# Optimization experiments

Measured on AMD Instinct MI355X. Metric: run time of the kernel, lower is better.

Reference implementation:

```python
import jax, jax.numpy as jnp
import numpy as np

B, S, D, H = 4, 2048, 1024, 16
DH = D // H  # 64

def setup_inputs() -> dict:
    key = jax.random.key(0)
    k0, k1, k2, k3 = jax.random.split(key, 4)
    x = jax.random.normal(k0, (B, S, D), dtype=jnp.float32)
    # Linear layers use random_normal init, shape (D, D), no bias.
    Wq = jax.random.normal(k1, (D, D), dtype=jnp.float32) * 0.05
    Wk = jax.random.normal(k2, (D, D), dtype=jnp.float32) * 0.05
    Wv = jax.random.normal(k3, (D, D), dtype=jnp.float32) * 0.05
    return {"encoder_input": x, "Wq": Wq, "Wk": Wk, "Wv": Wv}

def reference(encoder_input, Wq, Wk, Wv):
    x = encoder_input
    n_heads = H
    # Per-document projections, batched: [B,S,D]
    q = jnp.einsum('bsd,de->bse', x, Wq)
    k = jnp.einsum('bsd,de->bse', x, Wk)
    v = jnp.einsum('bsd,de->bse', x, Wv)
    # np.split(..., H, axis=-1) == reshape last dim to [H, DH]
    q = q.reshape(B, S, n_heads, DH)
    k = k.reshape(B, S, n_heads, DH)
    v = v.reshape(B, S, n_heads, DH)
    # Scaled dot-product attention; NOTE: original divides by N_HEADS, not sqrt(d_head)
    scores = jnp.einsum('bqhd,bkhd->bhqk', q, k) / jnp.float32(n_heads)
    attn = jax.nn.softmax(scores, axis=-1)
    out = jnp.einsum('bhqk,bkhd->bqhd', attn, v)
    # Concatenate heads along last dim -> [B,S,D]
    return out.reshape(B, S, D)
```

## Files before the change

kernel.cpp:

```cpp
#include <hip/hip_runtime.h>

typedef unsigned short u16;
typedef unsigned int   u32;
typedef __bf16 bf16x8 __attribute__((ext_vector_type(8)));
typedef __bf16 bf16x4 __attribute__((ext_vector_type(4)));
typedef float  f32x4  __attribute__((ext_vector_type(4)));
typedef u32    u32x4  __attribute__((ext_vector_type(4)));
typedef u32    u32x2  __attribute__((ext_vector_type(2)));
typedef u16    u16x8  __attribute__((ext_vector_type(8)));

#define MFMA16(a,b,c) __builtin_amdgcn_mfma_f32_16x16x32_bf16(a,b,c,0,0,0)

#define BB 4
#define SS 2048
#define DD 1024
#define HH 16
#define DH 64
#define MM 8192

#define QSCALE 0.0901684400555602f

#define WAIT_VM0() __builtin_amdgcn_s_waitcnt(0x0F70)

__device__ __forceinline__ u16 f2bf(float f) {
  u32 u = __builtin_bit_cast(u32, f);
  u += 0x7fffu + ((u >> 16) & 1u);
  return (u16)(u >> 16);
}

__device__ __forceinline__ void async16(const void* g, void* l) {
  __builtin_amdgcn_global_load_lds(
      (const __attribute__((address_space(1))) unsigned int*)g,
      (__attribute__((address_space(3))) unsigned int*)l, 16, 0, 0);
}

__global__ __launch_bounds__(256) void convert_x(
    const float* __restrict__ in, u16* __restrict__ out)
{
  const size_t stride = (size_t)gridDim.x * 256 * 8;
  for (size_t i = ((size_t)blockIdx.x * 256 + threadIdx.x) * 8;
       i < (size_t)MM * DD; i += stride) {
    f32x4 a = *(const f32x4*)(in + i);
    f32x4 b = *(const f32x4*)(in + i + 4);
    u32x2 ua = __builtin_bit_cast(u32x2, __builtin_convertvector(a, bf16x4));
    u32x2 ub = __builtin_bit_cast(u32x2, __builtin_convertvector(b, bf16x4));
    u32x4 v = {ua[0], ua[1], ub[0], ub[1]};
    *(u32x4*)(out + i) = v;
  }
}

__global__ __launch_bounds__(256) void fill_sig(float* __restrict__ out, int n)
{
  for (int i = blockIdx.x * 256 + threadIdx.x; i < n; i += gridDim.x * 256)
    out[i] = 3.0f;
}

__global__ __launch_bounds__(256) void convert_w(
    const float* __restrict__ w0, const float* __restrict__ w1,
    const float* __restrict__ w2, u16* __restrict__ WtAll)
{
  const int z = blockIdx.z;
  const float* W = (z == 0) ? w0 : ((z == 1) ? w1 : w2);
  u16* Wt = WtAll + (size_t)z * DD * DD;
  const int n0 = blockIdx.x * 64;
  const int k0 = blockIdx.y * 64;
  __shared__ u16 tile[64][65];
#pragma unroll
  for (int i = 0; i < 16; ++i) {
    int e = threadIdx.x + i * 256;
    int r = e >> 6, c = e & 63;
    tile[r][c] = f2bf(W[(size_t)(k0 + r) * DD + n0 + c]);
  }
  __syncthreads();
#pragma unroll
  for (int i = 0; i < 16; ++i) {
    int e = threadIdx.x + i * 256;
    int r = e >> 6, c = e & 63;
    Wt[(size_t)(n0 + r) * DD + k0 + c] = tile[c][r];
  }
}

__global__ __launch_bounds__(256) void qkv_gemm(
    const u16* __restrict__ X, const u16* __restrict__ WtAll,
    u16* __restrict__ QKV)
{
  const int z = blockIdx.z;
  const u16* Wt = WtAll + (size_t)z * DD * DD;
  u16* Y = QKV + (size_t)z * MM * DD;
  const int m0 = blockIdx.x * 128;
  const int n0 = blockIdx.y * 128;
  const int t = threadIdx.x;
  const int ln = t & 63;
  const int w  = t >> 6;
  const int cl = ln & 15;
  const int qd = ln >> 4;
  const int wm = (w & 1) * 64;
  const int wn = (w >> 1) * 64;
  const int srow8 = ln >> 3;
  const int sch   = (((ln & 7) ^ (srow8 & 7)) << 3);
  const int ch0   = ((qd ^ (cl & 7)) << 3);

  __shared__ __align__(16) u16 Asm[2][128 * 64];
  __shared__ __align__(16) u16 Bsm[2][128 * 64];

  const f32x4 fzero = {0.f, 0.f, 0.f, 0.f};
  f32x4 acc[4][4];
#pragma unroll
  for (int i = 0; i < 4; ++i)
#pragma unroll
    for (int j = 0; j < 4; ++j) acc[i][j] = fzero;

  auto stage = [&](int k0, int bi) {
#pragma unroll
    for (int c = 0; c < 4; ++c) {
      async16(X  + (size_t)(m0 + c * 32 + w * 8 + srow8) * DD + k0 + sch,
              &Asm[bi][(c * 32 + w * 8) * 64]);
      async16(Wt + (size_t)(n0 + c * 32 + w * 8 + srow8) * DD + k0 + sch,
              &Bsm[bi][(c * 32 + w * 8) * 64]);
    }
  };

  stage(0, 0);

  for (int k0 = 0; k0 < DD; k0 += 64) {
    const int cur = (k0 >> 6) & 1;
    WAIT_VM0();
    __syncthreads();
    if (k0 + 64 < DD) stage(k0 + 64, cur ^ 1);

    const u16* Ah = Asm[cur];
    const u16* Bh = Bsm[cur];

#pragma unroll
    for (int kk = 0; kk < 2; ++kk) {
      bf16x8 af[4], bf[4];
#pragma unroll
      for (int mb = 0; mb < 4; ++mb)
        af[mb] = *(const bf16x8*)&Ah[(wm + mb * 16 + cl) * 64 + (ch0 ^ (kk << 5))];
#pragma unroll
      for (int nb = 0; nb < 4; ++nb)
        bf[nb] = *(const bf16x8*)&Bh[(wn + nb * 16 + cl) * 64 + (ch0 ^ (kk << 5))];
#pragma unroll
      for (int mb = 0; mb < 4; ++mb)
#pragma unroll
        for (int nb = 0; nb < 4; ++nb)
          acc[mb][nb] = MFMA16(af[mb], bf[nb], acc[mb][nb]);
    }
  }

  const float scl = (z == 0) ? QSCALE : 1.0f;
#pragma unroll
  for (int mb = 0; mb < 4; ++mb) {
#pragma unroll
    for (int r = 0; r < 4; ++r) {
      const size_t row = (size_t)(m0 + wm + mb * 16 + qd * 4 + r) * DD;
      f32x4 v = {acc[mb][0][r] * scl, acc[mb][1][r] * scl,
                 acc[mb][2][r] * scl, acc[mb][3][r] * scl};
      bf16x4 bv = __builtin_convertvector(v, bf16x4);
#pragma unroll
      for (int nb = 0; nb < 4; ++nb)
        *(__bf16*)&Y[row + n0 + wn + nb * 16 + cl] = bv[nb];
    }
  }
}

__global__ __launch_bounds__(256) void vtrans(
    const u16* __restrict__ V, u16* __restrict__ VtG)
{
  const int b = blockIdx.z;
  const int h = blockIdx.y;
  const int s0 = blockIdx.x * 64;
  __shared__ u16 tile[64][65];
#pragma unroll
  for (int i = 0; i < 16; ++i) {
    int e = threadIdx.x + i * 256;
    int r = e >> 6, c = e & 63;
    tile[r][c] = V[(size_t)(b * SS + s0 + r) * DD + h * DH + c];
  }
  __syncthreads();
#pragma unroll
  for (int i = 0; i < 16; ++i) {
    int e = threadIdx.x + i * 256;
    int r = e >> 6, c = e & 63;
    int k = c & 31;
    int pos = (c & 32) + ((k & 15) >> 2) * 8 + (k >> 4) * 4 + (k & 3);
    VtG[((size_t)(b * HH + h) * DH + r) * SS + s0 + pos] = tile[c][r];
  }
}

__global__ __launch_bounds__(256, 2) void attn_kernel(
    const u16* __restrict__ QKV, const u16* __restrict__ VtG,
    float* __restrict__ Out)
{
  const int bh = blockIdx.x;
  const int b = bh >> 4;
  const int h = bh & 15;
  const int q0 = blockIdx.y * 256;
  const int t = threadIdx.x;
  const int ln = t & 63;
  const int w  = t >> 6;
  const int cl = ln & 15;
  const int qd = ln >> 4;
  const int srow = ln >> 2;
  const int swz = (((ln & 3) ^ ((srow >> 1) & 3)) << 3);
  const int sx = ((qd ^ ((cl >> 1) & 3)) << 3);

  const u16* Qg = QKV;
  const u16* Kg = QKV + (size_t)MM * DD;

  __shared__ __align__(16) u16 smem[16384];

  const size_t qoff0 = (size_t)(b * SS + q0 + w * 16 + cl) * DD + h * DH;
  const bf16x8 qf0a = *(const bf16x8*)(Qg + qoff0 + qd * 8);
  const bf16x8 qf0b = *(const bf16x8*)(Qg + qoff0 + 32 + qd * 8);
  const bf16x8 qf1a = *(const bf16x8*)(Qg + qoff0 + (size_t)64 * DD + qd * 8);
  const bf16x8 qf1b = *(const bf16x8*)(Qg + qoff0 + (size_t)64 * DD + 32 + qd * 8);
  const bf16x8 qf2a = *(const bf16x8*)(Qg + qoff0 + (size_t)128 * DD + qd * 8);
  const bf16x8 qf2b = *(const bf16x8*)(Qg + qoff0 + (size_t)128 * DD + 32 + qd * 8);
  const bf16x8 qf3a = *(const bf16x8*)(Qg + qoff0 + (size_t)192 * DD + qd * 8);
  const bf16x8 qf3b = *(const bf16x8*)(Qg + qoff0 + (size_t)192 * DD + 32 + qd * 8);

  const f32x4 fzero = {0.f, 0.f, 0.f, 0.f};
  f32x4 oacc0[4], oacc1[4], oacc2[4], oacc3[4];
#pragma unroll
  for (int mt = 0; mt < 4; ++mt) {
    oacc0[mt] = fzero; oacc1[mt] = fzero; oacc2[mt] = fzero; oacc3[mt] = fzero;
  }
  float lsum0 = 0.f, lsum1 = 0.f, lsum2 = 0.f, lsum3 = 0.f;

  const size_t kgbase  = (size_t)b * SS * DD + (size_t)h * DH;
  const size_t vtgbase = ((size_t)(b * HH + h)) * DH * SS;

  auto stage = [&](int kt, int bi) {
    u16* kb = smem + bi * 4096;
    u16* vb = smem + 8192 + bi * 4096;
#pragma unroll
    for (int s = 0; s < 2; ++s) {
      async16(Kg  + kgbase + (size_t)(kt + w * 16 + srow) * DD + s * 32 + swz,
              kb + (s * 64 + w * 16) * 32);
      async16(VtG + vtgbase + (size_t)(w * 16 + srow) * SS + kt + s * 32 + swz,
              vb + (s * 64 + w * 16) * 32);
    }
  };

#define PAIR(QA0, QA1, QB0, QB1, OA, OB, LA, LB) do {                         \
    f32x4 stA[4], stB[4];                                                     \
    _Pragma("unroll")                                                         \
    for (int mt = 0; mt < 4; ++mt) {                                          \
      f32x4 za = fzero, zb = fzero;                                           \
      za = MFMA16(kf0[mt], QA0, za); za = MFMA16(kf1[mt], QA1, za);           \
      zb = MFMA16(kf0[mt], QB0, zb); zb = MFMA16(kf1[mt], QB1, zb);           \
      stA[mt] = za; stB[mt] = zb;                                             \
    }                                                                         \
    f32x4 pa0, pa1, pa2, pa3;                                                 \
    _Pragma("unroll")                                                         \
    for (int r = 0; r < 4; ++r) {                                             \
      pa0[r] = __builtin_amdgcn_exp2f(stA[0][r]); LA += pa0[r];               \
      pa1[r] = __builtin_amdgcn_exp2f(stA[1][r]); LA += pa1[r];               \
      pa2[r] = __builtin_amdgcn_exp2f(stA[2][r]); LA += pa2[r];               \
      pa3[r] = __builtin_amdgcn_exp2f(stA[3][r]); LA += pa3[r];               \
    }                                                                         \
    {                                                                         \
      bf16x8 pf0 = __builtin_shufflevector(                                   \
          __builtin_convertvector(pa0, bf16x4),                               \
          __builtin_convertvector(pa1, bf16x4), 0, 1, 2, 3, 4, 5, 6, 7);      \
      bf16x8 pf1 = __builtin_shufflevector(                                   \
          __builtin_convertvector(pa2, bf16x4),                               \
          __builtin_convertvector(pa3, bf16x4), 0, 1, 2, 3, 4, 5, 6, 7);      \
      _Pragma("unroll")                                                       \
      for (int mt = 0; mt < 4; ++mt) {                                        \
        OA[mt] = MFMA16(vf0[mt], pf0, OA[mt]);                                \
        OA[mt] = MFMA16(vf1[mt], pf1, OA[mt]);                                \
      }                                                                       \
    }                                                                         \
    f32x4 pb0, pb1, pb2, pb3;                                                 \
    _Pragma("unroll")                                                         \
    for (int r = 0; r < 4; ++r) {                                             \
      pb0[r] = __builtin_amdgcn_exp2f(stB[0][r]); LB += pb0[r];               \
      pb1[r] = __builtin_amdgcn_exp2f(stB[1][r]); LB += pb1[r];               \
      pb2[r] = __builtin_amdgcn_exp2f(stB[2][r]); LB += pb2[r];               \
      pb3[r] = __builtin_amdgcn_exp2f(stB[3][r]); LB += pb3[r];               \
    }                                                                         \
    {                                                                         \
      bf16x8 pf0 = __builtin_shufflevector(                                   \
          __builtin_convertvector(pb0, bf16x4),                               \
          __builtin_convertvector(pb1, bf16x4), 0, 1, 2, 3, 4, 5, 6, 7);      \
      bf16x8 pf1 = __builtin_shufflevector(                                   \
          __builtin_convertvector(pb2, bf16x4),                               \
          __builtin_convertvector(pb3, bf16x4), 0, 1, 2, 3, 4, 5, 6, 7);      \
      _Pragma("unroll")                                                       \
      for (int mt = 0; mt < 4; ++mt) {                                        \
        OB[mt] = MFMA16(vf0[mt], pf0, OB[mt]);                                \
        OB[mt] = MFMA16(vf1[mt], pf1, OB[mt]);                                \
      }                                                                       \
    }                                                                         \
  } while (0)

  stage(0, 0);

  for (int it = 0; it < SS / 64; ++it) {
    const int cur = it & 1;
    WAIT_VM0();
    __syncthreads();
    if (it + 1 < SS / 64) stage((it + 1) * 64, cur ^ 1);

    const u16* Kh = smem + cur * 4096;
    const u16* Vh = smem + 8192 + cur * 4096;

    bf16x8 kf0[4], kf1[4], vf0[4], vf1[4];
#pragma unroll
    for (int mt = 0; mt < 4; ++mt) {
      kf0[mt] = *(const bf16x8*)&Kh[(mt * 16 + cl) * 32 + sx];
      kf1[mt] = *(const bf16x8*)&Kh[(64 + mt * 16 + cl) * 32 + sx];
      vf0[mt] = *(const bf16x8*)&Vh[(mt * 16 + cl) * 32 + sx];
      vf1[mt] = *(const bf16x8*)&Vh[(64 + mt * 16 + cl) * 32 + sx];
    }

    PAIR(qf0a, qf0b, qf1a, qf1b, oacc0, oacc1, lsum0, lsum1);
    PAIR(qf2a, qf2b, qf3a, qf3b, oacc2, oacc3, lsum2, lsum3);
  }

  lsum0 += __shfl_xor(lsum0, 16); lsum0 += __shfl_xor(lsum0, 32);
  lsum1 += __shfl_xor(lsum1, 16); lsum1 += __shfl_xor(lsum1, 32);
  lsum2 += __shfl_xor(lsum2, 16); lsum2 += __shfl_xor(lsum2, 32);
  lsum3 += __shfl_xor(lsum3, 16); lsum3 += __shfl_xor(lsum3, 32);

  __syncthreads();
  float* Ol = (float*)smem;
  const int q   = ln >> 2;
  const int seg = ln & 3;
  const float* src = Ol + w * 1088 + q * 68 + seg * 16;

#define EPI(OA, LS, SOFF) do {                                                \
    const float inv = 1.f / (LS);                                             \
    _Pragma("unroll")                                                         \
    for (int mt = 0; mt < 4; ++mt) {                                          \
      f32x4 vv = OA[mt];                                                      \
      _Pragma("unroll")                                                       \
      for (int r = 0; r < 4; ++r) vv[r] *= inv;                               \
      *(f32x4*)(Ol + w * 1088 + cl * 68 + mt * 16 + qd * 4) = vv;             \
    }                                                                         \
    {                                                                         \
      float* dst = Out + (size_t)(b * SS + q0 + (SOFF) + w * 16 + q) * DD     \
                       + h * DH + seg * 16;                                   \
      _Pragma("unroll")                                                       \
      for (int i = 0; i < 4; ++i)                                             \
        *(f32x4*)(dst + i * 4) = *(const f32x4*)(src + i * 4);                \
    }                                                                         \
  } while (0)

  EPI(oacc0, lsum0, 0);
  EPI(oacc1, lsum1, 64);
  EPI(oacc2, lsum2, 128);
  EPI(oacc3, lsum3, 192);

#undef EPI
#undef PAIR
}

extern "C" void kernel_launch(void* const* d_in, const int* in_sizes, int n_in,
                              void* d_out, int out_size, void* d_ws, size_t ws_size,
                              hipStream_t stream)
{
  const float* x  = (const float*)d_in[0];
  const float* wq = (const float*)d_in[1];
  const float* wk = (const float*)d_in[2];
  const float* wv = (const float*)d_in[3];
  float* out = (float*)d_out;

  const size_t need = ((size_t)MM * DD + 3 * (size_t)DD * DD +
                       3 * (size_t)MM * DD + (size_t)MM * DD) * sizeof(u16);
  if (ws_size < need) {
    fill_sig<<<1024, 256, 0, stream>>>(out, out_size);
    return;
  }

  u16* xs  = (u16*)d_ws;
  u16* wt  = xs + (size_t)MM * DD;
  u16* qkv = wt + (size_t)3 * DD * DD;
  u16* vtg = qkv + (size_t)3 * MM * DD;

  convert_x<<<2048, 256, 0, stream>>>(x, xs);
  convert_w<<<dim3(16, 16, 3), 256, 0, stream>>>(wq, wk, wv, wt);
  qkv_gemm<<<dim3(64, 8, 3), 256, 0, stream>>>(xs, wt, qkv);
  vtrans<<<dim3(32, HH, BB), 256, 0, stream>>>(qkv + (size_t)2 * MM * DD, vtg);
  attn_kernel<<<dim3(HH * BB, SS / 256, 1), 256, 0, stream>>>(qkv, vtg, out);
}
```

Baseline: 217.3 us.

## Enlarge QKV GEMM tile to 256x128 with triple-buffered LDS pipeline

```diff
diff --git a/kernel.cpp b/kernel.cpp
--- a/kernel.cpp
+++ b/kernel.cpp
@@ -80,28 +80,28 @@
   }
 }
 
-__global__ __launch_bounds__(256) void qkv_gemm(
+__global__ __launch_bounds__(512, 1) void qkv_gemm(
     const u16* __restrict__ X, const u16* __restrict__ WtAll,
     u16* __restrict__ QKV)
 {
   const int z = blockIdx.z;
   const u16* Wt = WtAll + (size_t)z * DD * DD;
   u16* Y = QKV + (size_t)z * MM * DD;
-  const int m0 = blockIdx.x * 128;
+  const int m0 = blockIdx.x * 256;
   const int n0 = blockIdx.y * 128;
   const int t = threadIdx.x;
   const int ln = t & 63;
   const int w  = t >> 6;
   const int cl = ln & 15;
   const int qd = ln >> 4;
-  const int wm = (w & 1) * 64;
-  const int wn = (w >> 1) * 64;
+  const int wm = (w >> 1) * 64;
+  const int wn = (w & 1) * 64;
   const int srow8 = ln >> 3;
-  const int sch   = (((ln & 7) ^ (srow8 & 7)) << 3);
+  const int sch   = (((ln & 7) ^ srow8) << 3);
   const int ch0   = ((qd ^ (cl & 7)) << 3);
 
-  __shared__ __align__(16) u16 Asm[2][128 * 64];
-  __shared__ __align__(16) u16 Bsm[2][128 * 64];
+  __shared__ __align__(16) u16 Asm[3][256 * 64];
+  __shared__ __align__(16) u16 Bsm[3][128 * 64];
 
   const f32x4 fzero = {0.f, 0.f, 0.f, 0.f};
   f32x4 acc[4][4];
@@ -110,23 +110,32 @@
 #pragma unroll
     for (int j = 0; j < 4; ++j) acc[i][j] = fzero;
 
-  auto stage = [&](int k0, int bi) {
-#pragma unroll
-    for (int c = 0; c < 4; ++c) {
-      async16(X  + (size_t)(m0 + c * 32 + w * 8 + srow8) * DD + k0 + sch,
-              &Asm[bi][(c * 32 + w * 8) * 64]);
-      async16(Wt + (size_t)(n0 + c * 32 + w * 8 + srow8) * DD + k0 + sch,
-              &Bsm[bi][(c * 32 + w * 8) * 64]);
+  auto stage = [&](int kt, int bi) {
+    const int k0 = kt * 64;
+#pragma unroll
+    for (int c = 0; c < 4; ++c)
+      async16(X + (size_t)(m0 + w * 32 + c * 8 + srow8) * DD + k0 + sch,
+              &Asm[bi][(w * 32 + c * 8) * 64]);
+#pragma unroll
+    for (int c = 0; c < 2; ++c)
+      async16(Wt + (size_t)(n0 + w * 16 + c * 8 + srow8) * DD + k0 + sch,
+              &Bsm[bi][(w * 16 + c * 8) * 64]);
+  };
+
+  stage(0, 0);
+  stage(1, 1);
+
+  const int NT = DD / 64;
+  int cur = 0, pre = 2;
+  for (int kt = 0; kt < NT; ++kt) {
+    if (kt + 1 < NT) {
+      asm volatile("s_waitcnt vmcnt(6)" ::: "memory");
+    } else {
+      asm volatile("s_waitcnt vmcnt(0)" ::: "memory");
     }
-  };
-
-  stage(0, 0);
-
-  for (int k0 = 0; k0 < DD; k0 += 64) {
-    const int cur = (k0 >> 6) & 1;
-    WAIT_VM0();
-    __syncthreads();
-    if (k0 + 64 < DD) stage(k0 + 64, cur ^ 1);
+    __builtin_amdgcn_s_barrier();
+    asm volatile("" ::: "memory");
+    if (kt + 2 < NT) stage(kt + 2, pre);
 
     const u16* Ah = Asm[cur];
     const u16* Bh = Bsm[cur];
@@ -140,12 +149,17 @@
 #pragma unroll
       for (int nb = 0; nb < 4; ++nb)
         bf[nb] = *(const bf16x8*)&Bh[(wn + nb * 16 + cl) * 64 + (ch0 ^ (kk << 5))];
+      __builtin_amdgcn_s_setprio(1);
 #pragma unroll
       for (int mb = 0; mb < 4; ++mb)
 #pragma unroll
         for (int nb = 0; nb < 4; ++nb)
           acc[mb][nb] = MFMA16(af[mb], bf[nb], acc[mb][nb]);
+      __builtin_amdgcn_s_setprio(0);
     }
+
+    cur = (cur == 2) ? 0 : cur + 1;
+    pre = (pre == 2) ? 0 : pre + 1;
   }
 
   const float scl = (z == 0) ? QSCALE : 1.0f;
@@ -382,7 +396,7 @@
 
   convert_x<<<2048, 256, 0, stream>>>(x, xs);
   convert_w<<<dim3(16, 16, 3), 256, 0, stream>>>(wq, wk, wv, wt);
-  qkv_gemm<<<dim3(64, 8, 3), 256, 0, stream>>>(xs, wt, qkv);
+  qkv_gemm<<<dim3(32, 8, 3), 512, 0, stream>>>(xs, wt, qkv);
   vtrans<<<dim3(32, HH, BB), 256, 0, stream>>>(qkv + (size_t)2 * MM * DD, vtg);
   attn_kernel<<<dim3(HH * BB, SS / 256, 1), 256, 0, stream>>>(qkv, vtg, out);
 }
```

New measurement: 234.6 us. 7.9% more time.

## Fuse V transpose into QKV GEMM epilogue and merge conversion kernels

Applied to the files above, without the earlier changes.

```diff
diff --git a/kernel.cpp b/kernel.cpp
--- a/kernel.cpp
+++ b/kernel.cpp
@@ -34,37 +34,38 @@
       (__attribute__((address_space(3))) unsigned int*)l, 16, 0, 0);
 }
 
-__global__ __launch_bounds__(256) void convert_x(
-    const float* __restrict__ in, u16* __restrict__ out)
-{
-  const size_t stride = (size_t)gridDim.x * 256 * 8;
-  for (size_t i = ((size_t)blockIdx.x * 256 + threadIdx.x) * 8;
-       i < (size_t)MM * DD; i += stride) {
-    f32x4 a = *(const f32x4*)(in + i);
-    f32x4 b = *(const f32x4*)(in + i + 4);
-    u32x2 ua = __builtin_bit_cast(u32x2, __builtin_convertvector(a, bf16x4));
-    u32x2 ub = __builtin_bit_cast(u32x2, __builtin_convertvector(b, bf16x4));
-    u32x4 v = {ua[0], ua[1], ub[0], ub[1]};
-    *(u32x4*)(out + i) = v;
-  }
-}
-
 __global__ __launch_bounds__(256) void fill_sig(float* __restrict__ out, int n)
 {
   for (int i = blockIdx.x * 256 + threadIdx.x; i < n; i += gridDim.x * 256)
     out[i] = 3.0f;
 }
 
-__global__ __launch_bounds__(256) void convert_w(
+__global__ __launch_bounds__(256) void prep(
+    const float* __restrict__ x,
     const float* __restrict__ w0, const float* __restrict__ w1,
-    const float* __restrict__ w2, u16* __restrict__ WtAll)
+    const float* __restrict__ w2,
+    u16* __restrict__ xs, u16* __restrict__ WtAll)
 {
   const int z = blockIdx.z;
+  __shared__ u16 tile[64][65];
+  if (z == 3) {
+    const int blk = blockIdx.x + blockIdx.y * 16;
+    const size_t stride = (size_t)256 * 256 * 8;
+    for (size_t i = ((size_t)blk * 256 + threadIdx.x) * 8;
+         i < (size_t)MM * DD; i += stride) {
+      f32x4 a = *(const f32x4*)(x + i);
+      f32x4 b = *(const f32x4*)(x + i + 4);
+      u32x2 ua = __builtin_bit_cast(u32x2, __builtin_convertvector(a, bf16x4));
+      u32x2 ub = __builtin_bit_cast(u32x2, __builtin_convertvector(b, bf16x4));
+      u32x4 v = {ua[0], ua[1], ub[0], ub[1]};
+      *(u32x4*)(xs + i) = v;
+    }
+    return;
+  }
   const float* W = (z == 0) ? w0 : ((z == 1) ? w1 : w2);
   u16* Wt = WtAll + (size_t)z * DD * DD;
   const int n0 = blockIdx.x * 64;
   const int k0 = blockIdx.y * 64;
-  __shared__ u16 tile[64][65];
 #pragma unroll
   for (int i = 0; i < 16; ++i) {
     int e = threadIdx.x + i * 256;
@@ -82,7 +83,7 @@
 
 __global__ __launch_bounds__(256) void qkv_gemm(
     const u16* __restrict__ X, const u16* __restrict__ WtAll,
-    u16* __restrict__ QKV)
+    u16* __restrict__ QKV, u16* __restrict__ VtG)
 {
   const int z = blockIdx.z;
   const u16* Wt = WtAll + (size_t)z * DD * DD;
@@ -148,43 +149,45 @@
     }
   }
 
-  const float scl = (z == 0) ? QSCALE : 1.0f;
-#pragma unroll
-  for (int mb = 0; mb < 4; ++mb) {
-#pragma unroll
-    for (int r = 0; r < 4; ++r) {
-      const size_t row = (size_t)(m0 + wm + mb * 16 + qd * 4 + r) * DD;
-      f32x4 v = {acc[mb][0][r] * scl, acc[mb][1][r] * scl,
-                 acc[mb][2][r] * scl, acc[mb][3][r] * scl};
-      bf16x4 bv = __builtin_convertvector(v, bf16x4);
-#pragma unroll
-      for (int nb = 0; nb < 4; ++nb)
-        *(__bf16*)&Y[row + n0 + wn + nb * 16 + cl] = bv[nb];
-    }
-  }
-}
-
-__global__ __launch_bounds__(256) void vtrans(
-    const u16* __restrict__ V, u16* __restrict__ VtG)
-{
-  const int b = blockIdx.z;
-  const int h = blockIdx.y;
-  const int s0 = blockIdx.x * 64;
-  __shared__ u16 tile[64][65];
-#pragma unroll
-  for (int i = 0; i < 16; ++i) {
-    int e = threadIdx.x + i * 256;
-    int r = e >> 6, c = e & 63;
-    tile[r][c] = V[(size_t)(b * SS + s0 + r) * DD + h * DH + c];
-  }
-  __syncthreads();
-#pragma unroll
-  for (int i = 0; i < 16; ++i) {
-    int e = threadIdx.x + i * 256;
-    int r = e >> 6, c = e & 63;
-    int k = c & 31;
-    int pos = (c & 32) + ((k & 15) >> 2) * 8 + (k >> 4) * 4 + (k & 3);
-    VtG[((size_t)(b * HH + h) * DH + r) * SS + s0 + pos] = tile[c][r];
+  if (z < 2) {
+    const float scl = (z == 0) ? QSCALE : 1.0f;
+#pragma unroll
+    for (int mb = 0; mb < 4; ++mb) {
+#pragma unroll
+      for (int r = 0; r < 4; ++r) {
+        const size_t row = (size_t)(m0 + wm + mb * 16 + qd * 4 + r) * DD;
+        f32x4 v = {acc[mb][0][r] * scl, acc[mb][1][r] * scl,
+                   acc[mb][2][r] * scl, acc[mb][3][r] * scl};
+        bf16x4 bv = __builtin_convertvector(v, bf16x4);
+#pragma unroll
+        for (int nb = 0; nb < 4; ++nb)
+          *(__bf16*)&Y[row + n0 + wn + nb * 16 + cl] = bv[nb];
+      }
+    }
+  } else {
+    __syncthreads();
+    u16* slab = (u16*)Asm + w * 4096;
+    const int bb = m0 >> 11;
+    const int hh = (n0 + wn) >> 6;
+    const int S0 = m0 - bb * SS + wm;
+#pragma unroll
+    for (int mb = 0; mb < 4; ++mb) {
+      const int sp = (mb >> 1) * 32 + qd * 8 + (mb & 1) * 4;
+#pragma unroll
+      for (int nb = 0; nb < 4; ++nb) {
+        f32x4 v = {acc[mb][nb][0], acc[mb][nb][1],
+                   acc[mb][nb][2], acc[mb][nb][3]};
+        bf16x4 bv = __builtin_convertvector(v, bf16x4);
+        *(bf16x4*)&slab[(nb * 16 + cl) * 64 + sp] = bv;
+      }
+    }
+    const size_t vbase = ((size_t)(bb * HH + hh)) * DH * SS;
+#pragma unroll
+    for (int i = 0; i < 8; ++i) {
+      const int dr = (ln >> 3) + i * 8;
+      const u16x8 vv = *(const u16x8*)&slab[dr * 64 + (ln & 7) * 8];
+      *(u16x8*)(VtG + vbase + (size_t)dr * SS + S0 + (ln & 7) * 8) = vv;
+    }
   }
 }
 
@@ -380,9 +383,7 @@
   u16* qkv = wt + (size_t)3 * DD * DD;
   u16* vtg = qkv + (size_t)3 * MM * DD;
 
-  convert_x<<<2048, 256, 0, stream>>>(x, xs);
-  convert_w<<<dim3(16, 16, 3), 256, 0, stream>>>(wq, wk, wv, wt);
-  qkv_gemm<<<dim3(64, 8, 3), 256, 0, stream>>>(xs, wt, qkv);
-  vtrans<<<dim3(32, HH, BB), 256, 0, stream>>>(qkv + (size_t)2 * MM * DD, vtg);
+  prep<<<dim3(16, 16, 4), 256, 0, stream>>>(x, wq, wk, wv, xs, wt);
+  qkv_gemm<<<dim3(64, 8, 3), 256, 0, stream>>>(xs, wt, qkv, vtg);
   attn_kernel<<<dim3(HH * BB, SS / 256, 1), 256, 0, stream>>>(qkv, vtg, out);
 }
```

New measurement: 220.3 us. No clear change (+1.4%).
